# Performance work log

Hardware: AMD Instinct MI355X
Metric: run time of the kernel (lower is better)

The kernel has to match this reference:

```python
import jax, jax.numpy as jnp
import numpy as np

H = 128      # hidden_size
B = 8192     # number of sessions
L = 50       # items per session (constant here; code supports ragged)
T = B * L    # total tokens


def setup_inputs() -> dict:
    key = jax.random.key(0)
    ks = jax.random.split(key, 10)
    s = 1.0 / np.sqrt(H)
    u = lambda k, shape: jax.random.uniform(k, shape, jnp.float32, -s, s)
    return {
        "intra_item_emb": jax.random.normal(ks[0], (T, H), jnp.float32),
        "inter_item_emb": jax.random.normal(ks[1], (T, H), jnp.float32),
        "W1": u(ks[2], (H, H)), "b1": u(ks[3], (H,)),
        "W2": u(ks[4], (H, H)), "b2": u(ks[5], (H,)),
        "q_w": u(ks[6], (1, H)), "q_b": u(ks[7], (1,)),
        "W3": u(ks[8], (H, 2 * H)), "b3": u(ks[9], (H,)),
        "seq_len": jnp.full((B,), L, dtype=jnp.int32),
    }


def reference(intra_item_emb, inter_item_emb, W1, b1, W2, b2, q_w, q_b, W3, b3, seq_len):
    # max_fusing: elementwise max of the two embedding streams  [T, H]
    hidden = jnp.maximum(intra_item_emb, inter_item_emb)
    nB = seq_len.shape[0]
    nT = hidden.shape[0]
    # segment id per token and index of last token of each session
    seg_ids = jnp.repeat(jnp.arange(nB), seq_len, total_repeat_length=nT)  # [T]
    last_idx = jnp.cumsum(seq_len) - 1                                      # [B]
    v_n = hidden[last_idx]                 # [B, H] last node of each session
    v_n_rep = v_n[seg_ids]                 # [T, H] broadcast last node to tokens
    # attention weight per token: q(sigmoid(W1 v_n + W2 h))  [T, 1]
    alpha = jax.nn.sigmoid(v_n_rep @ W1.T + b1 + hidden @ W2.T + b2) @ q_w.T + q_b
    # segment-sum pooling of alpha-weighted tokens  [B, H]
    s_g = jax.ops.segment_sum(alpha * hidden, seg_ids, num_segments=nB)
    # final session representation  [B, H]
    h_s = jnp.concatenate([v_n, s_g], axis=1) @ W3.T + b3
    return h_s
```

## Files before the change

### kernel.cpp

```cpp
#include <hip/hip_runtime.h>
#include <hip/hip_bf16.h>

#define HDIM 128
#define RS 136

typedef __attribute__((ext_vector_type(8))) short short8;
typedef __attribute__((ext_vector_type(4))) float floatv4;

__device__ __forceinline__ unsigned short f2bf(float f) {
  union { float f; unsigned u; } x; x.f = f;
  unsigned r = x.u + 0x7fffu + ((x.u >> 16) & 1u);
  return (unsigned short)(r >> 16);
}
__device__ __forceinline__ float blo(unsigned u) { return __uint_as_float(u << 16); }
__device__ __forceinline__ float bhi(unsigned u) { return __uint_as_float(u & 0xffff0000u); }

__device__ __forceinline__ float dot8(const unsigned short* w, const float* v) {
  uint4 u = *(const uint4*)w;
  return blo(u.x) * v[0] + bhi(u.x) * v[1] + blo(u.y) * v[2] + bhi(u.y) * v[3] +
         blo(u.z) * v[4] + bhi(u.z) * v[5] + blo(u.w) * v[6] + bhi(u.w) * v[7];
}

__global__ void scan_kernel(const int* __restrict__ seq, int* __restrict__ offs, int B) {
  __shared__ int part[256];
  int tid = threadIdx.x;
  int chunk = (B + 255) >> 8;
  int beg = tid * chunk, end = min(beg + chunk, B);
  int s = 0;
  for (int i = beg; i < end; ++i) s += seq[i];
  part[tid] = s;
  __syncthreads();
  for (int d = 1; d < 256; d <<= 1) {
    int v = (tid >= d) ? part[tid - d] : 0;
    __syncthreads();
    part[tid] += v;
    __syncthreads();
  }
  int run = (tid == 0) ? 0 : part[tid - 1];
  for (int i = beg; i < end; ++i) { offs[i] = run; run += seq[i]; }
}

__global__ void convert_kernel(const float* __restrict__ W1, const float* __restrict__ W2,
                               const float* __restrict__ W3,
                               unsigned short* __restrict__ w1b, unsigned short* __restrict__ w2b,
                               unsigned short* __restrict__ w3b) {
  int i = blockIdx.x * blockDim.x + threadIdx.x;
  if (i < 16384) { w1b[i] = f2bf(W1[i]); w2b[i] = f2bf(W2[i]); }
  if (i < 32768) { w3b[i] = f2bf(W3[i]); }
}

__global__ __launch_bounds__(256) void session_kernel(
    const float* __restrict__ intra, const float* __restrict__ inter,
    const unsigned short* __restrict__ w1b, const float* __restrict__ b1,
    const unsigned short* __restrict__ w2b, const float* __restrict__ b2,
    const float* __restrict__ qw, const float* __restrict__ qb,
    const unsigned short* __restrict__ w3b, const float* __restrict__ b3,
    const int* __restrict__ seq, const int* __restrict__ offs,
    float* __restrict__ out) {
  __shared__ unsigned short hbf[64 * RS];
  __shared__ float vn[HDIM], cvec[HDIM], qv[HDIM], sg[HDIM];
  __shared__ float alphaAcc[64];
  __shared__ float sgpart[2][HDIM];

  const int b = blockIdx.x;
  const int tid = threadIdx.x;
  int n = seq[b];
  const int start = offs[b];
  if (n > 64) n = 64;

  {
    int last = start + n - 1;
    if (last < 0) last = 0;
    if (tid < HDIM) {
      size_t base = (size_t)last * HDIM + tid;
      vn[tid] = fmaxf(intra[base], inter[base]);
      qv[tid] = qw[tid];
    }
    if (tid < 64) alphaAcc[tid] = qb[0];
  }

  for (int it = 0; it < 8; ++it) {
    int e = (it << 10) + (tid << 2);
    int t = e >> 7, j = e & 127;
    float r0 = 0.f, r1 = 0.f, r2 = 0.f, r3 = 0.f;
    if (t < n) {
      const float4 a = *(const float4*)(intra + (size_t)(start + t) * HDIM + j);
      const float4 c = *(const float4*)(inter + (size_t)(start + t) * HDIM + j);
      r0 = fmaxf(a.x, c.x); r1 = fmaxf(a.y, c.y);
      r2 = fmaxf(a.z, c.z); r3 = fmaxf(a.w, c.w);
    }
    ushort4 p; p.x = f2bf(r0); p.y = f2bf(r1); p.z = f2bf(r2); p.w = f2bf(r3);
    *(ushort4*)&hbf[t * RS + j] = p;
  }
  __syncthreads();

  {
    int j = tid >> 1, h = tid & 1;
    const unsigned short* wr = w1b + j * HDIM + (h << 6);
    const float* v = vn + (h << 6);
    float s = 0.f;
    #pragma unroll
    for (int i = 0; i < 64; i += 8) s += dot8(wr + i, v + i);
    s += __shfl_xor(s, 1, 64);
    if (h == 0) cvec[j] = s + b1[j] + b2[j];
  }

  const int lane = tid & 63, wid = tid >> 6;
  const int quad = lane >> 4, lcol = lane & 15;
  const int nbase = wid << 5;
  short8 bfrag[2][4];
  #pragma unroll
  for (int nt = 0; nt < 2; ++nt) {
    int nn = nbase + (nt << 4) + lcol;
    #pragma unroll
    for (int kt = 0; kt < 4; ++kt)
      bfrag[nt][kt] = *(const short8*)(w2b + nn * HDIM + (kt << 5) + (quad << 3));
  }
  __syncthreads();

  #pragma unroll
  for (int mt = 0; mt < 4; ++mt) {
    floatv4 acc0 = {0.f, 0.f, 0.f, 0.f}, acc1 = {0.f, 0.f, 0.f, 0.f};
    const unsigned short* arow = &hbf[((mt << 4) + lcol) * RS + (quad << 3)];
    #pragma unroll
    for (int kt = 0; kt < 4; ++kt) {
      short8 af = *(const short8*)(arow + (kt << 5));
      acc0 = __builtin_amdgcn_mfma_f32_16x16x32_bf16(af, bfrag[0][kt], acc0, 0, 0, 0);
      acc1 = __builtin_amdgcn_mfma_f32_16x16x32_bf16(af, bfrag[1][kt], acc1, 0, 0, 0);
    }
    float c0 = cvec[nbase + lcol], c1 = cvec[nbase + 16 + lcol];
    float q0 = qv[nbase + lcol], q1 = qv[nbase + 16 + lcol];
    #pragma unroll
    for (int r = 0; r < 4; ++r) {
      float v = q0 / (1.f + __expf(-(c0 + acc0[r])))
              + q1 / (1.f + __expf(-(c1 + acc1[r])));
      v += __shfl_xor(v, 1, 64);
      v += __shfl_xor(v, 2, 64);
      v += __shfl_xor(v, 4, 64);
      v += __shfl_xor(v, 8, 64);
      if (lcol == 0) atomicAdd(&alphaAcc[(mt << 4) + (quad << 2) + r], v);
    }
  }
  __syncthreads();

  {
    int j = tid & 127, h = tid >> 7;
    int t0 = h << 5, t1 = min(n, t0 + 32);
    float acc = 0.f;
    for (int t = t0; t < t1; ++t)
      acc += alphaAcc[t] * __uint_as_float((unsigned)hbf[t * RS + j] << 16);
    sgpart[h][j] = acc;
  }
  __syncthreads();
  if (tid < HDIM) sg[tid] = sgpart[0][tid] + sgpart[1][tid];
  __syncthreads();

  {
    int i = tid >> 1, h = tid & 1;
    const unsigned short* wr = w3b + i * 256 + (h << 7);
    const float* src = h ? sg : vn;
    float s = 0.f;
    #pragma unroll
    for (int k = 0; k < HDIM; k += 8) s += dot8(wr + k, src + k);
    s += __shfl_xor(s, 1, 64);
    if (h == 0) out[(size_t)b * HDIM + i] = s + b3[i];
  }
}

extern "C" void kernel_launch(void* const* d_in, const int* in_sizes, int n_in,
                              void* d_out, int out_size, void* d_ws, size_t ws_size,
                              hipStream_t stream) {
  const float* intra = (const float*)d_in[0];
  const float* inter = (const float*)d_in[1];
  const float* W1 = (const float*)d_in[2];
  const float* b1 = (const float*)d_in[3];
  const float* W2 = (const float*)d_in[4];
  const float* b2 = (const float*)d_in[5];
  const float* qw = (const float*)d_in[6];
  const float* qb = (const float*)d_in[7];
  const float* W3 = (const float*)d_in[8];
  const float* b3 = (const float*)d_in[9];
  const int* seq = (const int*)d_in[10];
  const int B = in_sizes[10];
  float* out = (float*)d_out;

  char* ws = (char*)d_ws;
  size_t o1 = (((size_t)B * 4) + 255) & ~(size_t)255;
  int* offs = (int*)ws;
  unsigned short* w1b = (unsigned short*)(ws + o1);
  unsigned short* w2b = (unsigned short*)(ws + o1 + 32768);
  unsigned short* w3b = (unsigned short*)(ws + o1 + 65536);

  hipLaunchKernelGGL(scan_kernel, dim3(1), dim3(256), 0, stream, seq, offs, B);
  hipLaunchKernelGGL(convert_kernel, dim3(128), dim3(256), 0, stream, W1, W2, W3, w1b, w2b, w3b);
  hipLaunchKernelGGL(session_kernel, dim3(B), dim3(256), 0, stream,
                     intra, inter, w1b, b1, w2b, b2, qw, qb, w3b, b3, seq, offs, out);
}
```

Before: 539.9 us.

## Move session matvecs to MFMA, vectorize pooling, merge prep kernels

The W1 and W3 matrix-vector products now run on bf16 MFMA instructions instead of per-thread scalar dot products. The last-node vector is kept in bf16 in shared memory, and the W1 result plus biases seeds the W2 accumulators directly, which drops the cvec buffer and one barrier. Alpha-weighted pooling now uses 16-byte LDS reads and wave shuffles across four partial buffers. The sigmoid division becomes a hardware reciprocal, and the scan and weight-conversion kernels are merged into one launch. The cost is extra bf16 rounding on the last-node and pooled vectors before the W3 product.

```diff
diff --git a/kernel.cpp b/kernel.cpp
--- a/kernel.cpp
+++ b/kernel.cpp
@@ -7,46 +7,41 @@
 typedef __attribute__((ext_vector_type(8))) short short8;
 typedef __attribute__((ext_vector_type(4))) float floatv4;
 
-__device__ __forceinline__ unsigned short f2bf(float f) {
+static __device__ __forceinline__ unsigned short f2bf(float f) {
   union { float f; unsigned u; } x; x.f = f;
   unsigned r = x.u + 0x7fffu + ((x.u >> 16) & 1u);
   return (unsigned short)(r >> 16);
 }
-__device__ __forceinline__ float blo(unsigned u) { return __uint_as_float(u << 16); }
-__device__ __forceinline__ float bhi(unsigned u) { return __uint_as_float(u & 0xffff0000u); }
-
-__device__ __forceinline__ float dot8(const unsigned short* w, const float* v) {
-  uint4 u = *(const uint4*)w;
-  return blo(u.x) * v[0] + bhi(u.x) * v[1] + blo(u.y) * v[2] + bhi(u.y) * v[3] +
-         blo(u.z) * v[4] + bhi(u.z) * v[5] + blo(u.w) * v[6] + bhi(u.w) * v[7];
-}
-
-__global__ void scan_kernel(const int* __restrict__ seq, int* __restrict__ offs, int B) {
-  __shared__ int part[256];
-  int tid = threadIdx.x;
-  int chunk = (B + 255) >> 8;
-  int beg = tid * chunk, end = min(beg + chunk, B);
-  int s = 0;
-  for (int i = beg; i < end; ++i) s += seq[i];
-  part[tid] = s;
-  __syncthreads();
-  for (int d = 1; d < 256; d <<= 1) {
-    int v = (tid >= d) ? part[tid - d] : 0;
+static __device__ __forceinline__ float blo(unsigned u) { return __uint_as_float(u << 16); }
+static __device__ __forceinline__ float bhi(unsigned u) { return __uint_as_float(u & 0xffff0000u); }
+
+__global__ void prep_kernel(const int* __restrict__ seq, int* __restrict__ offs, int B,
+                            const float* __restrict__ W1, const float* __restrict__ W2,
+                            const float* __restrict__ W3,
+                            unsigned short* __restrict__ w1b, unsigned short* __restrict__ w2b,
+                            unsigned short* __restrict__ w3b) {
+  if (blockIdx.x == 0) {
+    __shared__ int part[256];
+    int tid = threadIdx.x;
+    int chunk = (B + 255) >> 8;
+    int beg = tid * chunk, end = min(beg + chunk, B);
+    int s = 0;
+    for (int i = beg; i < end; ++i) s += seq[i];
+    part[tid] = s;
     __syncthreads();
-    part[tid] += v;
-    __syncthreads();
-  }
-  int run = (tid == 0) ? 0 : part[tid - 1];
-  for (int i = beg; i < end; ++i) { offs[i] = run; run += seq[i]; }
-}
-
-__global__ void convert_kernel(const float* __restrict__ W1, const float* __restrict__ W2,
-                               const float* __restrict__ W3,
-                               unsigned short* __restrict__ w1b, unsigned short* __restrict__ w2b,
-                               unsigned short* __restrict__ w3b) {
-  int i = blockIdx.x * blockDim.x + threadIdx.x;
-  if (i < 16384) { w1b[i] = f2bf(W1[i]); w2b[i] = f2bf(W2[i]); }
-  if (i < 32768) { w3b[i] = f2bf(W3[i]); }
+    for (int d = 1; d < 256; d <<= 1) {
+      int v = (tid >= d) ? part[tid - d] : 0;
+      __syncthreads();
+      part[tid] += v;
+      __syncthreads();
+    }
+    int run = (tid == 0) ? 0 : part[tid - 1];
+    for (int i = beg; i < end; ++i) { offs[i] = run; run += seq[i]; }
+  } else {
+    int i = (blockIdx.x - 1) * 256 + threadIdx.x;
+    if (i < 16384) { w1b[i] = f2bf(W1[i]); w2b[i] = f2bf(W2[i]); }
+    if (i < 32768) { w3b[i] = f2bf(W3[i]); }
+  }
 }
 
 __global__ __launch_bounds__(256) void session_kernel(
@@ -58,82 +53,91 @@
     const int* __restrict__ seq, const int* __restrict__ offs,
     float* __restrict__ out) {
   __shared__ unsigned short hbf[64 * RS];
-  __shared__ float vn[HDIM], cvec[HDIM], qv[HDIM], sg[HDIM];
+  __shared__ unsigned short vnb[HDIM];
+  __shared__ unsigned short sgb[HDIM];
   __shared__ float alphaAcc[64];
-  __shared__ float sgpart[2][HDIM];
+  __shared__ float sgpart[4][HDIM];
 
   const int b = blockIdx.x;
   const int tid = threadIdx.x;
+  const int lane = tid & 63, wid = tid >> 6;
+  const int quad = lane >> 4, lcol = lane & 15;
+  const int nbase = wid << 5;
+  const int n0 = nbase + lcol, n1 = n0 + 16;
+
   int n = seq[b];
   const int start = offs[b];
   if (n > 64) n = 64;
 
-  {
+  if (tid < HDIM) {
     int last = start + n - 1;
     if (last < 0) last = 0;
-    if (tid < HDIM) {
-      size_t base = (size_t)last * HDIM + tid;
-      vn[tid] = fmaxf(intra[base], inter[base]);
-      qv[tid] = qw[tid];
-    }
-    if (tid < 64) alphaAcc[tid] = qb[0];
-  }
-
-  for (int it = 0; it < 8; ++it) {
-    int e = (it << 10) + (tid << 2);
-    int t = e >> 7, j = e & 127;
-    float r0 = 0.f, r1 = 0.f, r2 = 0.f, r3 = 0.f;
-    if (t < n) {
-      const float4 a = *(const float4*)(intra + (size_t)(start + t) * HDIM + j);
-      const float4 c = *(const float4*)(inter + (size_t)(start + t) * HDIM + j);
-      r0 = fmaxf(a.x, c.x); r1 = fmaxf(a.y, c.y);
-      r2 = fmaxf(a.z, c.z); r3 = fmaxf(a.w, c.w);
-    }
-    ushort4 p; p.x = f2bf(r0); p.y = f2bf(r1); p.z = f2bf(r2); p.w = f2bf(r3);
-    *(ushort4*)&hbf[t * RS + j] = p;
-  }
-  __syncthreads();
-
-  {
-    int j = tid >> 1, h = tid & 1;
-    const unsigned short* wr = w1b + j * HDIM + (h << 6);
-    const float* v = vn + (h << 6);
-    float s = 0.f;
-    #pragma unroll
-    for (int i = 0; i < 64; i += 8) s += dot8(wr + i, v + i);
-    s += __shfl_xor(s, 1, 64);
-    if (h == 0) cvec[j] = s + b1[j] + b2[j];
-  }
-
-  const int lane = tid & 63, wid = tid >> 6;
-  const int quad = lane >> 4, lcol = lane & 15;
-  const int nbase = wid << 5;
-  short8 bfrag[2][4];
+    size_t base = (size_t)last * HDIM + tid;
+    vnb[tid] = f2bf(fmaxf(intra[base], inter[base]));
+  }
+  if (tid < 64) alphaAcc[tid] = qb[0];
+
+  {
+    const float4* pa = (const float4*)(intra + (size_t)start * HDIM);
+    const float4* pb = (const float4*)(inter + (size_t)start * HDIM);
+    #pragma unroll
+    for (int it = 0; it < 8; ++it) {
+      int idx = (it << 8) + tid;
+      int t = idx >> 5, j4 = idx & 31;
+      float4 r; r.x = 0.f; r.y = 0.f; r.z = 0.f; r.w = 0.f;
+      if (t < n) {
+        float4 a = pa[idx], c = pb[idx];
+        r.x = fmaxf(a.x, c.x); r.y = fmaxf(a.y, c.y);
+        r.z = fmaxf(a.z, c.z); r.w = fmaxf(a.w, c.w);
+      }
+      union { __hip_bfloat162 b; unsigned u; } p01, p23;
+      p01.b = __float22bfloat162_rn(make_float2(r.x, r.y));
+      p23.b = __float22bfloat162_rn(make_float2(r.z, r.w));
+      uint2 st; st.x = p01.u; st.y = p23.u;
+      *(uint2*)&hbf[t * RS + (j4 << 2)] = st;
+    }
+  }
+
+  short8 w2f[2][4];
   #pragma unroll
   for (int nt = 0; nt < 2; ++nt) {
     int nn = nbase + (nt << 4) + lcol;
     #pragma unroll
     for (int kt = 0; kt < 4; ++kt)
-      bfrag[nt][kt] = *(const short8*)(w2b + nn * HDIM + (kt << 5) + (quad << 3));
-  }
-  __syncthreads();
+      w2f[nt][kt] = *(const short8*)(w2b + nn * HDIM + (kt << 5) + (quad << 3));
+  }
+  __syncthreads();
+
+  float c0, c1;
+  {
+    floatv4 p0 = {0.f, 0.f, 0.f, 0.f}, p1 = {0.f, 0.f, 0.f, 0.f};
+    #pragma unroll
+    for (int kt = 0; kt < 4; ++kt) {
+      short8 af = *(const short8*)&vnb[(kt << 5) + (quad << 3)];
+      short8 bf0 = *(const short8*)(w1b + n0 * HDIM + (kt << 5) + (quad << 3));
+      short8 bf1 = *(const short8*)(w1b + n1 * HDIM + (kt << 5) + (quad << 3));
+      p0 = __builtin_amdgcn_mfma_f32_16x16x32_bf16(af, bf0, p0, 0, 0, 0);
+      p1 = __builtin_amdgcn_mfma_f32_16x16x32_bf16(af, bf1, p1, 0, 0, 0);
+    }
+    c0 = p0[0] + b1[n0] + b2[n0];
+    c1 = p1[0] + b1[n1] + b2[n1];
+  }
+  const float q0 = qw[n0], q1 = qw[n1];
 
   #pragma unroll
   for (int mt = 0; mt < 4; ++mt) {
-    floatv4 acc0 = {0.f, 0.f, 0.f, 0.f}, acc1 = {0.f, 0.f, 0.f, 0.f};
+    floatv4 a0 = {c0, c0, c0, c0}, a1 = {c1, c1, c1, c1};
     const unsigned short* arow = &hbf[((mt << 4) + lcol) * RS + (quad << 3)];
     #pragma unroll
     for (int kt = 0; kt < 4; ++kt) {
       short8 af = *(const short8*)(arow + (kt << 5));
-      acc0 = __builtin_amdgcn_mfma_f32_16x16x32_bf16(af, bfrag[0][kt], acc0, 0, 0, 0);
-      acc1 = __builtin_amdgcn_mfma_f32_16x16x32_bf16(af, bfrag[1][kt], acc1, 0, 0, 0);
-    }
-    float c0 = cvec[nbase + lcol], c1 = cvec[nbase + 16 + lcol];
-    float q0 = qv[nbase + lcol], q1 = qv[nbase + 16 + lcol];
+      a0 = __builtin_amdgcn_mfma_f32_16x16x32_bf16(af, w2f[0][kt], a0, 0, 0, 0);
+      a1 = __builtin_amdgcn_mfma_f32_16x16x32_bf16(af, w2f[1][kt], a1, 0, 0, 0);
+    }
     #pragma unroll
     for (int r = 0; r < 4; ++r) {
-      float v = q0 / (1.f + __expf(-(c0 + acc0[r])))
-              + q1 / (1.f + __expf(-(c1 + acc1[r])));
+      float v = q0 * __builtin_amdgcn_rcpf(1.f + __expf(-a0[r]))
+              + q1 * __builtin_amdgcn_rcpf(1.f + __expf(-a1[r]));
       v += __shfl_xor(v, 1, 64);
       v += __shfl_xor(v, 2, 64);
       v += __shfl_xor(v, 4, 64);
@@ -144,26 +148,54 @@
   __syncthreads();
 
   {
-    int j = tid & 127, h = tid >> 7;
-    int t0 = h << 5, t1 = min(n, t0 + 32);
-    float acc = 0.f;
-    for (int t = t0; t < t1; ++t)
-      acc += alphaAcc[t] * __uint_as_float((unsigned)hbf[t * RS + j] << 16);
-    sgpart[h][j] = acc;
-  }
-  __syncthreads();
-  if (tid < HDIM) sg[tid] = sgpart[0][tid] + sgpart[1][tid];
-  __syncthreads();
-
-  {
-    int i = tid >> 1, h = tid & 1;
-    const unsigned short* wr = w3b + i * 256 + (h << 7);
-    const float* src = h ? sg : vn;
-    float s = 0.f;
-    #pragma unroll
-    for (int k = 0; k < HDIM; k += 8) s += dot8(wr + k, src + k);
-    s += __shfl_xor(s, 1, 64);
-    if (h == 0) out[(size_t)b * HDIM + i] = s + b3[i];
+    int jg = tid & 15, ts = tid >> 4;
+    float ac[8];
+    #pragma unroll
+    for (int e = 0; e < 8; ++e) ac[e] = 0.f;
+    #pragma unroll
+    for (int tt = 0; tt < 4; ++tt) {
+      int t = (tt << 4) + ts;
+      float al = alphaAcc[t];
+      uint4 u = *(const uint4*)&hbf[t * RS + (jg << 3)];
+      ac[0] += al * blo(u.x); ac[1] += al * bhi(u.x);
+      ac[2] += al * blo(u.y); ac[3] += al * bhi(u.y);
+      ac[4] += al * blo(u.z); ac[5] += al * bhi(u.z);
+      ac[6] += al * blo(u.w); ac[7] += al * bhi(u.w);
+    }
+    #pragma unroll
+    for (int e = 0; e < 8; ++e) {
+      ac[e] += __shfl_xor(ac[e], 16, 64);
+      ac[e] += __shfl_xor(ac[e], 32, 64);
+    }
+    if (quad == 0) {
+      float4 s0; s0.x = ac[0]; s0.y = ac[1]; s0.z = ac[2]; s0.w = ac[3];
+      float4 s1; s1.x = ac[4]; s1.y = ac[5]; s1.z = ac[6]; s1.w = ac[7];
+      *(float4*)&sgpart[wid][(jg << 3)] = s0;
+      *(float4*)&sgpart[wid][(jg << 3) + 4] = s1;
+    }
+  }
+  __syncthreads();
+  if (tid < HDIM) {
+    float s = sgpart[0][tid] + sgpart[1][tid] + sgpart[2][tid] + sgpart[3][tid];
+    sgb[tid] = f2bf(s);
+  }
+  __syncthreads();
+
+  {
+    floatv4 o0 = {0.f, 0.f, 0.f, 0.f}, o1 = {0.f, 0.f, 0.f, 0.f};
+    #pragma unroll
+    for (int kt = 0; kt < 8; ++kt) {
+      const unsigned short* src = (kt < 4) ? &vnb[kt << 5] : &sgb[(kt - 4) << 5];
+      short8 af = *(const short8*)(src + (quad << 3));
+      short8 bf0 = *(const short8*)(w3b + n0 * 256 + (kt << 5) + (quad << 3));
+      short8 bf1 = *(const short8*)(w3b + n1 * 256 + (kt << 5) + (quad << 3));
+      o0 = __builtin_amdgcn_mfma_f32_16x16x32_bf16(af, bf0, o0, 0, 0, 0);
+      o1 = __builtin_amdgcn_mfma_f32_16x16x32_bf16(af, bf1, o1, 0, 0, 0);
+    }
+    if (quad == 0) {
+      out[(size_t)b * HDIM + n0] = o0[0] + b3[n0];
+      out[(size_t)b * HDIM + n1] = o1[0] + b3[n1];
+    }
   }
 }
 
@@ -191,8 +223,8 @@
   unsigned short* w2b = (unsigned short*)(ws + o1 + 32768);
   unsigned short* w3b = (unsigned short*)(ws + o1 + 65536);
 
-  hipLaunchKernelGGL(scan_kernel, dim3(1), dim3(256), 0, stream, seq, offs, B);
-  hipLaunchKernelGGL(convert_kernel, dim3(128), dim3(256), 0, stream, W1, W2, W3, w1b, w2b, w3b);
+  hipLaunchKernelGGL(prep_kernel, dim3(129), dim3(256), 0, stream,
+                     seq, offs, B, W1, W2, W3, w1b, w2b, w3b);
   hipLaunchKernelGGL(session_kernel, dim3(B), dim3(256), 0, stream,
                      intra, inter, w1b, b1, w2b, b2, qw, qb, w3b, b3, seq, offs, out);
 }
```

Result: faster. 507.6 us (-6.0%).
